# Optimization experiments

Hardware: AMD Instinct MI355X
Metric: run time of the kernel (lower is better)

The kernel has to match this reference:

```python
import jax, jax.numpy as jnp
import numpy as np

N_EMBD = 1024
N_HEAD = 16
HEAD_DIM = N_EMBD // N_HEAD
MASK_FILL = -10.0  # module uses -10, not -inf


def setup_inputs() -> dict:
    key = jax.random.key(0)
    kx, kq, kk, kv, ko = jax.random.split(key, 5)
    B, T = 4, 2048
    s = 1.0 / np.sqrt(N_EMBD)
    return {
        "x": jax.random.normal(kx, (B, T, N_EMBD), dtype=jnp.float32),
        "wq": jax.random.normal(kq, (N_EMBD, N_EMBD), dtype=jnp.float32) * s,
        "wk": jax.random.normal(kk, (N_EMBD, N_EMBD), dtype=jnp.float32) * s,
        "wv": jax.random.normal(kv, (N_EMBD, N_EMBD), dtype=jnp.float32) * s,
        "wo": jax.random.normal(ko, (N_EMBD, N_EMBD), dtype=jnp.float32) * s,
    }


def reference(x, wq, wk, wv, wo):
    B, T, C = x.shape
    # nn.Linear applies x @ W.T; weights here stored as [out, in]
    q = (x @ wq.T).reshape(B, T, N_HEAD, HEAD_DIM).transpose(0, 2, 1, 3)
    k = (x @ wk.T).reshape(B, T, N_HEAD, HEAD_DIM).transpose(0, 2, 1, 3)
    v = (x @ wv.T).reshape(B, T, N_HEAD, HEAD_DIM).transpose(0, 2, 1, 3)
    scale = 1.0 / np.sqrt(HEAD_DIM)
    att = jnp.einsum("bhqd,bhkd->bhqk", q, k) * scale  # [B,H,T,T]
    causal = jnp.tril(jnp.ones((T, T), dtype=bool))
    att = jnp.where(causal[None, None, :, :], att, MASK_FILL)
    att = jax.nn.softmax(att, axis=-1)
    y = jnp.einsum("bhqk,bhkd->bhqd", att, v)
    y = y.transpose(0, 2, 1, 3).reshape(B, T, C)
    return y @ wo.T
```

## Files before the change

kernel.cpp:

```cpp
#include <hip/hip_runtime.h>

typedef __attribute__((ext_vector_type(8))) short bf16x8;
typedef __attribute__((ext_vector_type(4))) float f32x4;

#define T_SEQ 2048
#define EXPM10 4.5399929762484854e-05f

__device__ __forceinline__ unsigned short f2bf(float f) {
    unsigned int u = __builtin_bit_cast(unsigned int, f);
    u += 0x7fffu + ((u >> 16) & 1u);
    return (unsigned short)(u >> 16);
}
__device__ __forceinline__ float bf2f(unsigned short u) {
    return __builtin_bit_cast(float, (unsigned int)u << 16);
}

__device__ __forceinline__ void async16(void* lds, const void* g) {
    __builtin_amdgcn_global_load_lds(
        (__attribute__((address_space(1))) void*)g,
        (__attribute__((address_space(3))) void*)lds, 16, 0, 0);
}

__global__ __launch_bounds__(256) void cvt_bf16(const float* __restrict__ src,
                                                unsigned short* __restrict__ dst, int n4) {
    int i = blockIdx.x * 256 + threadIdx.x;
    if (i < n4) {
        float4 v = ((const float4*)src)[i];
        ushort4 r;
        r.x = f2bf(v.x); r.y = f2bf(v.y); r.z = f2bf(v.z); r.w = f2bf(v.w);
        ((ushort4*)dst)[i] = r;
    }
}

__global__ __launch_bounds__(256) void cvt_w(const float* __restrict__ wq,
                                             const float* __restrict__ wk,
                                             const float* __restrict__ wv,
                                             const float* __restrict__ wo,
                                             unsigned short* __restrict__ wqkv,
                                             unsigned short* __restrict__ wob) {
    int which = blockIdx.x >> 10;
    int i = (blockIdx.x & 1023) * 256 + threadIdx.x;
    const float* src = which == 0 ? wq : which == 1 ? wk : which == 2 ? wv : wo;
    unsigned short* dst = which < 3 ? wqkv + (size_t)which * 1048576 : wob;
    float4 v = ((const float4*)src)[i];
    ushort4 r;
    r.x = f2bf(v.x); r.y = f2bf(v.y); r.z = f2bf(v.z); r.w = f2bf(v.w);
    ((ushort4*)dst)[i] = r;
}

__global__ __launch_bounds__(256) void gemm_qkv(const unsigned short* __restrict__ A,
                                                const unsigned short* __restrict__ B,
                                                unsigned short* __restrict__ Qb,
                                                unsigned short* __restrict__ Kb,
                                                unsigned short* __restrict__ Vtb) {
    __shared__ unsigned short As[128 * 32];
    __shared__ unsigned short Bs[128 * 32];
    const int K = 1024;
    int m0 = blockIdx.y * 128, n0 = blockIdx.x * 128;
    int tid = threadIdx.x;
    int wave = tid >> 6, lane = tid & 63;
    int r = lane & 15, q = lane >> 4;
    int wr = wave >> 1, wc = wave & 1;

    f32x4 acc[4][4];
#pragma unroll
    for (int i = 0; i < 4; i++)
#pragma unroll
        for (int j = 0; j < 4; j++) acc[i][j] = (f32x4){0.f, 0.f, 0.f, 0.f};

    for (int k0 = 0; k0 < K; k0 += 32) {
#pragma unroll
        for (int i = 0; i < 2; i++) {
            int li = i * 256 + tid;
            int row = li >> 2, kk = (li & 3) << 3;
            async16(&As[i * 2048 + wave * 512], &A[(size_t)(m0 + row) * K + k0 + kk]);
            async16(&Bs[i * 2048 + wave * 512], &B[(size_t)(n0 + row) * K + k0 + kk]);
        }
        __syncthreads();
        bf16x8 af[4], bfr[4];
#pragma unroll
        for (int mi = 0; mi < 4; mi++)
            af[mi] = *(const bf16x8*)&As[(wr * 64 + mi * 16 + r) * 32 + q * 8];
#pragma unroll
        for (int ni = 0; ni < 4; ni++)
            bfr[ni] = *(const bf16x8*)&Bs[(wc * 64 + ni * 16 + r) * 32 + q * 8];
#pragma unroll
        for (int mi = 0; mi < 4; mi++)
#pragma unroll
            for (int ni = 0; ni < 4; ni++)
                acc[mi][ni] = __builtin_amdgcn_mfma_f32_16x16x32_bf16(
                    af[mi], bfr[ni], acc[mi][ni], 0, 0, 0);
        __syncthreads();
    }

#pragma unroll
    for (int mi = 0; mi < 4; mi++) {
#pragma unroll
        for (int ni = 0; ni < 4; ni++) {
#pragma unroll
            for (int rr = 0; rr < 4; rr++) {
                int gm = m0 + wr * 64 + mi * 16 + q * 4 + rr;
                int gn = n0 + wc * 64 + ni * 16 + r;
                float v = acc[mi][ni][rr];
                int b = gm >> 11, t = gm & 2047;
                int sel = gn >> 10, nn = gn & 1023;
                int h = nn >> 6, d = nn & 63;
                if (sel == 0)
                    Qb[((size_t)(b * 16 + h) * 2048 + t) * 64 + d] = f2bf(v);
                else if (sel == 1)
                    Kb[((size_t)(b * 16 + h) * 2048 + t) * 64 + d] = f2bf(v);
                else
                    Vtb[((size_t)(b * 16 + h) * 64 + d) * 2048 + t] = f2bf(v);
            }
        }
    }
}

__global__ __launch_bounds__(256) void gemm_out(const unsigned short* __restrict__ A,
                                                const unsigned short* __restrict__ B,
                                                float* __restrict__ out) {
    __shared__ unsigned short As[128 * 32];
    __shared__ unsigned short Bs[128 * 32];
    const int K = 1024;
    int m0 = blockIdx.y * 128, n0 = blockIdx.x * 128;
    int tid = threadIdx.x;
    int wave = tid >> 6, lane = tid & 63;
    int r = lane & 15, q = lane >> 4;
    int wr = wave >> 1, wc = wave & 1;

    f32x4 acc[4][4];
#pragma unroll
    for (int i = 0; i < 4; i++)
#pragma unroll
        for (int j = 0; j < 4; j++) acc[i][j] = (f32x4){0.f, 0.f, 0.f, 0.f};

    for (int k0 = 0; k0 < K; k0 += 32) {
#pragma unroll
        for (int i = 0; i < 2; i++) {
            int li = i * 256 + tid;
            int row = li >> 2, kk = (li & 3) << 3;
            async16(&As[i * 2048 + wave * 512], &A[(size_t)(m0 + row) * K + k0 + kk]);
            async16(&Bs[i * 2048 + wave * 512], &B[(size_t)(n0 + row) * K + k0 + kk]);
        }
        __syncthreads();
        bf16x8 af[4], bfr[4];
#pragma unroll
        for (int mi = 0; mi < 4; mi++)
            af[mi] = *(const bf16x8*)&As[(wr * 64 + mi * 16 + r) * 32 + q * 8];
#pragma unroll
        for (int ni = 0; ni < 4; ni++)
            bfr[ni] = *(const bf16x8*)&Bs[(wc * 64 + ni * 16 + r) * 32 + q * 8];
#pragma unroll
        for (int mi = 0; mi < 4; mi++)
#pragma unroll
            for (int ni = 0; ni < 4; ni++)
                acc[mi][ni] = __builtin_amdgcn_mfma_f32_16x16x32_bf16(
                    af[mi], bfr[ni], acc[mi][ni], 0, 0, 0);
        __syncthreads();
    }

#pragma unroll
    for (int mi = 0; mi < 4; mi++)
#pragma unroll
        for (int ni = 0; ni < 4; ni++)
#pragma unroll
            for (int rr = 0; rr < 4; rr++) {
                int gm = m0 + wr * 64 + mi * 16 + q * 4 + rr;
                int gn = n0 + wc * 64 + ni * 16 + r;
                out[(size_t)gm * 1024 + gn] = acc[mi][ni][rr];
            }
}

__global__ __launch_bounds__(256) void suffix_sv(const unsigned short* __restrict__ Vt,
                                                 float* __restrict__ SV) {
    __shared__ float bsum[32][64];
    int bh = blockIdx.x;
    int d = threadIdx.x & 63, c = threadIdx.x >> 6;
    const unsigned short* base = Vt + ((size_t)bh * 64 + d) * T_SEQ;
#pragma unroll
    for (int jj = 0; jj < 8; jj++) {
        int j = c * 8 + jj;
        float s = 0.f;
#pragma unroll
        for (int t8 = 0; t8 < 8; t8++) {
            bf16x8 v = *(const bf16x8*)(base + j * 64 + t8 * 8);
#pragma unroll
            for (int e = 0; e < 8; e++) s += bf2f((unsigned short)v[e]);
        }
        bsum[j][d] = s;
    }
    __syncthreads();
    if (threadIdx.x < 64) {
        float run = 0.f;
        for (int j = 31; j >= 0; j--) {
            run += bsum[j][d];
            SV[((size_t)bh * 32 + j) * 64 + d] = run;
        }
    }
}

#define KST 72
#define VST 72
#define PST 72
__global__ __launch_bounds__(256) void attn(const unsigned short* __restrict__ Q,
                                            const unsigned short* __restrict__ Kg,
                                            const unsigned short* __restrict__ Vt,
                                            const float* __restrict__ SV,
                                            unsigned short* __restrict__ Y) {
    __shared__ unsigned short Ks[64 * KST];
    __shared__ unsigned short Vs[64 * VST];
    __shared__ unsigned short Ps[4][16 * PST];
    int bh = blockIdx.y;
    int qi = 31 - blockIdx.x;
    int q0 = qi * 64;
    int tid = threadIdx.x, wave = tid >> 6, lane = tid & 63;
    int r = lane & 15, qd = lane >> 4;
    int query = q0 + wave * 16 + r;

    const unsigned short* qptr = Q + ((size_t)bh * T_SEQ + query) * 64 + qd * 8;
    bf16x8 qf0 = *(const bf16x8*)qptr;
    bf16x8 qf1 = *(const bf16x8*)(qptr + 32);

    float l_lane = 0.0f;
    f32x4 o[4];
#pragma unroll
    for (int n = 0; n < 4; n++) o[n] = (f32x4){0.f, 0.f, 0.f, 0.f};

    int srow = tid >> 2, scol = (tid & 3) * 16;
    const unsigned short* kg = Kg + ((size_t)bh * T_SEQ + srow) * 64 + scol;
    const unsigned short* vg = Vt + ((size_t)bh * 64 + srow) * T_SEQ + scol;
    const float scale = 0.125f;

    bf16x8 pk0 = *(const bf16x8*)(kg);
    bf16x8 pk1 = *(const bf16x8*)(kg + 8);
    bf16x8 pv0 = *(const bf16x8*)(vg);
    bf16x8 pv1 = *(const bf16x8*)(vg + 8);

    int iters = qi + 1;
    for (int it = 0; it < iters; ++it) {
        __syncthreads();
        *(bf16x8*)&Ks[srow * KST + scol]     = pk0;
        *(bf16x8*)&Ks[srow * KST + scol + 8] = pk1;
        *(bf16x8*)&Vs[srow * VST + scol]     = pv0;
        *(bf16x8*)&Vs[srow * VST + scol + 8] = pv1;
        __syncthreads();
        if (it + 1 < iters) {
            size_t kn = (size_t)(it + 1) * 64;
            pk0 = *(const bf16x8*)(kg + kn * 64);
            pk1 = *(const bf16x8*)(kg + kn * 64 + 8);
            pv0 = *(const bf16x8*)(vg + kn);
            pv1 = *(const bf16x8*)(vg + kn + 8);
        }

        int k0 = it * 64;
        f32x4 st[4];
#pragma unroll
        for (int t = 0; t < 4; t++) {
            bf16x8 kf0 = *(const bf16x8*)&Ks[(t * 16 + r) * KST + qd * 8];
            bf16x8 kf1 = *(const bf16x8*)&Ks[(t * 16 + r) * KST + 32 + qd * 8];
            st[t] = (f32x4){0.f, 0.f, 0.f, 0.f};
            st[t] = __builtin_amdgcn_mfma_f32_16x16x32_bf16(kf0, qf0, st[t], 0, 0, 0);
            st[t] = __builtin_amdgcn_mfma_f32_16x16x32_bf16(kf1, qf1, st[t], 0, 0, 0);
        }

        float p[4][4], sum = 0.f;
        bool anymask = (k0 + 63 > q0 + wave * 16);
        if (anymask) {
#pragma unroll
            for (int t = 0; t < 4; t++)
#pragma unroll
                for (int e = 0; e < 4; e++) {
                    int kgidx = k0 + t * 16 + qd * 4 + e;
                    float pe = __expf(st[t][e] * scale);
                    p[t][e] = (kgidx <= query) ? pe : EXPM10;
                    sum += p[t][e];
                }
        } else {
#pragma unroll
            for (int t = 0; t < 4; t++)
#pragma unroll
                for (int e = 0; e < 4; e++) {
                    p[t][e] = __expf(st[t][e] * scale);
                    sum += p[t][e];
                }
        }
        l_lane += sum;

#pragma unroll
        for (int t = 0; t < 4; t++) {
            ushort4 pk;
            pk.x = f2bf(p[t][0]); pk.y = f2bf(p[t][1]);
            pk.z = f2bf(p[t][2]); pk.w = f2bf(p[t][3]);
            *(ushort4*)&Ps[wave][r * PST + t * 16 + qd * 4] = pk;
        }
        __builtin_amdgcn_sched_barrier(0);

        bf16x8 pf0 = *(const bf16x8*)&Ps[wave][r * PST + qd * 8];
        bf16x8 pf1 = *(const bf16x8*)&Ps[wave][r * PST + 32 + qd * 8];
#pragma unroll
        for (int n = 0; n < 4; n++) {
            bf16x8 vf0 = *(const bf16x8*)&Vs[(n * 16 + r) * VST + qd * 8];
            bf16x8 vf1 = *(const bf16x8*)&Vs[(n * 16 + r) * VST + 32 + qd * 8];
            o[n] = __builtin_amdgcn_mfma_f32_16x16x32_bf16(vf0, pf0, o[n], 0, 0, 0);
            o[n] = __builtin_amdgcn_mfma_f32_16x16x32_bf16(vf1, pf1, o[n], 0, 0, 0);
        }
    }

    float l_i = l_lane;
    l_i += __shfl_xor(l_i, 16);
    l_i += __shfl_xor(l_i, 32);

    float pm = 0.f, tail_l = 0.f;
    float sv[4][4];
#pragma unroll
    for (int n = 0; n < 4; n++)
#pragma unroll
        for (int e = 0; e < 4; e++) sv[n][e] = 0.f;
    if (qi < 31) {
        pm = EXPM10;
        tail_l = (float)(T_SEQ - 64 * (qi + 1)) * pm;
        const float* svp = SV + ((size_t)bh * 32 + qi + 1) * 64;
#pragma unroll
        for (int n = 0; n < 4; n++) {
            float4 f = *(const float4*)(svp + n * 16 + qd * 4);
            sv[n][0] = f.x; sv[n][1] = f.y; sv[n][2] = f.z; sv[n][3] = f.w;
        }
    }
    float inv = 1.0f / (l_i + tail_l);
    int b = bh >> 4, h = bh & 15;
#pragma unroll
    for (int n = 0; n < 4; n++) {
        ushort4 yk;
        yk.x = f2bf((o[n][0] + pm * sv[n][0]) * inv);
        yk.y = f2bf((o[n][1] + pm * sv[n][1]) * inv);
        yk.z = f2bf((o[n][2] + pm * sv[n][2]) * inv);
        yk.w = f2bf((o[n][3] + pm * sv[n][3]) * inv);
        *(ushort4*)&Y[(((size_t)b * T_SEQ + query) * 16 + h) * 64 + n * 16 + qd * 4] = yk;
    }
}

extern "C" void kernel_launch(void* const* d_in, const int* in_sizes, int n_in,
                              void* d_out, int out_size, void* d_ws, size_t ws_size,
                              hipStream_t stream) {
    const float* x  = (const float*)d_in[0];
    const float* wq = (const float*)d_in[1];
    const float* wk = (const float*)d_in[2];
    const float* wv = (const float*)d_in[3];
    const float* wo = (const float*)d_in[4];

    char* ws = (char*)d_ws;
    const size_t MB = 1u << 20;
    unsigned short* xb   = (unsigned short*)(ws);
    unsigned short* Qb   = (unsigned short*)(ws + 16 * MB);
    unsigned short* Kb   = (unsigned short*)(ws + 32 * MB);
    unsigned short* Vtb  = (unsigned short*)(ws + 48 * MB);
    unsigned short* wqkv = (unsigned short*)(ws + 64 * MB);
    unsigned short* wob  = (unsigned short*)(ws + 70 * MB);
    unsigned short* Yb   = xb;
    float* SVf = (float*)d_out;

    cvt_bf16<<<8192, 256, 0, stream>>>(x, xb, 2097152);
    cvt_w<<<4096, 256, 0, stream>>>(wq, wk, wv, wo, wqkv, wob);

    gemm_qkv<<<dim3(24, 64), 256, 0, stream>>>(xb, wqkv, Qb, Kb, Vtb);

    suffix_sv<<<64, 256, 0, stream>>>(Vtb, SVf);

    attn<<<dim3(32, 64), 256, 0, stream>>>(Qb, Kb, Vtb, SVf, Yb);

    gemm_out<<<dim3(8, 64), 256, 0, stream>>>(Yb, wob, (float*)d_out);
}
```

Measured before the change: 349.6 us.

## Double query tile per attention block and widen GEMM K-step to 64

The attention kernel now processes 128 queries per block as two 64-query groups, so each K/V tile loaded into shared memory serves twice as many queries. This halves the grid and reuses K/V staging, with the first group skipping the final diagonal tile. Both GEMMs now stage two 32-wide K slices per barrier pair, halving synchronisation count. The trade-offs are more registers and LDS per block, and fewer blocks for the causal attention grid, which can hurt occupancy and load balance.

```diff
diff --git a/kernel.cpp b/kernel.cpp
--- a/kernel.cpp
+++ b/kernel.cpp
@@ -53,8 +53,8 @@
                                                 unsigned short* __restrict__ Qb,
                                                 unsigned short* __restrict__ Kb,
                                                 unsigned short* __restrict__ Vtb) {
-    __shared__ unsigned short As[128 * 32];
-    __shared__ unsigned short Bs[128 * 32];
+    __shared__ unsigned short As[2][4096];
+    __shared__ unsigned short Bs[2][4096];
     const int K = 1024;
     int m0 = blockIdx.y * 128, n0 = blockIdx.x * 128;
     int tid = threadIdx.x;
@@ -68,28 +68,34 @@
 #pragma unroll
         for (int j = 0; j < 4; j++) acc[i][j] = (f32x4){0.f, 0.f, 0.f, 0.f};
 
-    for (int k0 = 0; k0 < K; k0 += 32) {
-#pragma unroll
-        for (int i = 0; i < 2; i++) {
-            int li = i * 256 + tid;
-            int row = li >> 2, kk = (li & 3) << 3;
-            async16(&As[i * 2048 + wave * 512], &A[(size_t)(m0 + row) * K + k0 + kk]);
-            async16(&Bs[i * 2048 + wave * 512], &B[(size_t)(n0 + row) * K + k0 + kk]);
-        }
-        __syncthreads();
-        bf16x8 af[4], bfr[4];
-#pragma unroll
-        for (int mi = 0; mi < 4; mi++)
-            af[mi] = *(const bf16x8*)&As[(wr * 64 + mi * 16 + r) * 32 + q * 8];
-#pragma unroll
-        for (int ni = 0; ni < 4; ni++)
-            bfr[ni] = *(const bf16x8*)&Bs[(wc * 64 + ni * 16 + r) * 32 + q * 8];
-#pragma unroll
-        for (int mi = 0; mi < 4; mi++)
+    int row = tid >> 2, kk = (tid & 3) << 3;
+    for (int k0 = 0; k0 < K; k0 += 64) {
+#pragma unroll
+        for (int s = 0; s < 2; s++)
+#pragma unroll
+            for (int i = 0; i < 2; i++) {
+                int li = i * 256 + tid;
+                int rw = li >> 2, kc = (li & 3) << 3;
+                async16(&As[s][i * 2048 + wave * 512], &A[(size_t)(m0 + rw) * K + k0 + s * 32 + kc]);
+                async16(&Bs[s][i * 2048 + wave * 512], &B[(size_t)(n0 + rw) * K + k0 + s * 32 + kc]);
+            }
+        __syncthreads();
+#pragma unroll
+        for (int s = 0; s < 2; s++) {
+            bf16x8 af[4], bfr[4];
+#pragma unroll
+            for (int mi = 0; mi < 4; mi++)
+                af[mi] = *(const bf16x8*)&As[s][(wr * 64 + mi * 16 + r) * 32 + q * 8];
 #pragma unroll
             for (int ni = 0; ni < 4; ni++)
-                acc[mi][ni] = __builtin_amdgcn_mfma_f32_16x16x32_bf16(
-                    af[mi], bfr[ni], acc[mi][ni], 0, 0, 0);
+                bfr[ni] = *(const bf16x8*)&Bs[s][(wc * 64 + ni * 16 + r) * 32 + q * 8];
+#pragma unroll
+            for (int mi = 0; mi < 4; mi++)
+#pragma unroll
+                for (int ni = 0; ni < 4; ni++)
+                    acc[mi][ni] = __builtin_amdgcn_mfma_f32_16x16x32_bf16(
+                        af[mi], bfr[ni], acc[mi][ni], 0, 0, 0);
+        }
         __syncthreads();
     }
 
@@ -119,8 +125,8 @@
 __global__ __launch_bounds__(256) void gemm_out(const unsigned short* __restrict__ A,
                                                 const unsigned short* __restrict__ B,
                                                 float* __restrict__ out) {
-    __shared__ unsigned short As[128 * 32];
-    __shared__ unsigned short Bs[128 * 32];
+    __shared__ unsigned short As[2][4096];
+    __shared__ unsigned short Bs[2][4096];
     const int K = 1024;
     int m0 = blockIdx.y * 128, n0 = blockIdx.x * 128;
     int tid = threadIdx.x;
@@ -134,28 +140,33 @@
 #pragma unroll
         for (int j = 0; j < 4; j++) acc[i][j] = (f32x4){0.f, 0.f, 0.f, 0.f};
 
-    for (int k0 = 0; k0 < K; k0 += 32) {
-#pragma unroll
-        for (int i = 0; i < 2; i++) {
-            int li = i * 256 + tid;
-            int row = li >> 2, kk = (li & 3) << 3;
-            async16(&As[i * 2048 + wave * 512], &A[(size_t)(m0 + row) * K + k0 + kk]);
-            async16(&Bs[i * 2048 + wave * 512], &B[(size_t)(n0 + row) * K + k0 + kk]);
-        }
-        __syncthreads();
-        bf16x8 af[4], bfr[4];
-#pragma unroll
-        for (int mi = 0; mi < 4; mi++)
-            af[mi] = *(const bf16x8*)&As[(wr * 64 + mi * 16 + r) * 32 + q * 8];
-#pragma unroll
-        for (int ni = 0; ni < 4; ni++)
-            bfr[ni] = *(const bf16x8*)&Bs[(wc * 64 + ni * 16 + r) * 32 + q * 8];
-#pragma unroll
-        for (int mi = 0; mi < 4; mi++)
+    for (int k0 = 0; k0 < K; k0 += 64) {
+#pragma unroll
+        for (int s = 0; s < 2; s++)
+#pragma unroll
+            for (int i = 0; i < 2; i++) {
+                int li = i * 256 + tid;
+                int rw = li >> 2, kc = (li & 3) << 3;
+                async16(&As[s][i * 2048 + wave * 512], &A[(size_t)(m0 + rw) * K + k0 + s * 32 + kc]);
+                async16(&Bs[s][i * 2048 + wave * 512], &B[(size_t)(n0 + rw) * K + k0 + s * 32 + kc]);
+            }
+        __syncthreads();
+#pragma unroll
+        for (int s = 0; s < 2; s++) {
+            bf16x8 af[4], bfr[4];
+#pragma unroll
+            for (int mi = 0; mi < 4; mi++)
+                af[mi] = *(const bf16x8*)&As[s][(wr * 64 + mi * 16 + r) * 32 + q * 8];
 #pragma unroll
             for (int ni = 0; ni < 4; ni++)
-                acc[mi][ni] = __builtin_amdgcn_mfma_f32_16x16x32_bf16(
-                    af[mi], bfr[ni], acc[mi][ni], 0, 0, 0);
+                bfr[ni] = *(const bf16x8*)&Bs[s][(wc * 64 + ni * 16 + r) * 32 + q * 8];
+#pragma unroll
+            for (int mi = 0; mi < 4; mi++)
+#pragma unroll
+                for (int ni = 0; ni < 4; ni++)
+                    acc[mi][ni] = __builtin_amdgcn_mfma_f32_16x16x32_bf16(
+                        af[mi], bfr[ni], acc[mi][ni], 0, 0, 0);
+        }
         __syncthreads();
     }
 
@@ -209,35 +220,42 @@
                                             unsigned short* __restrict__ Y) {
     __shared__ unsigned short Ks[64 * KST];
     __shared__ unsigned short Vs[64 * VST];
-    __shared__ unsigned short Ps[4][16 * PST];
+    __shared__ unsigned short Ps[8 * 16 * PST];
     int bh = blockIdx.y;
-    int qi = 31 - blockIdx.x;
-    int q0 = qi * 64;
+    int qi = 15 - blockIdx.x;
+    int q0 = qi * 128;
     int tid = threadIdx.x, wave = tid >> 6, lane = tid & 63;
     int r = lane & 15, qd = lane >> 4;
-    int query = q0 + wave * 16 + r;
-
-    const unsigned short* qptr = Q + ((size_t)bh * T_SEQ + query) * 64 + qd * 8;
-    bf16x8 qf0 = *(const bf16x8*)qptr;
-    bf16x8 qf1 = *(const bf16x8*)(qptr + 32);
-
-    float l_lane = 0.0f;
-    f32x4 o[4];
-#pragma unroll
-    for (int n = 0; n < 4; n++) o[n] = (f32x4){0.f, 0.f, 0.f, 0.f};
+    int query0 = q0 + wave * 16 + r;
+    int query1 = query0 + 64;
+
+    const unsigned short* qptr = Q + ((size_t)bh * T_SEQ + query0) * 64 + qd * 8;
+    bf16x8 qf00 = *(const bf16x8*)qptr;
+    bf16x8 qf01 = *(const bf16x8*)(qptr + 32);
+    bf16x8 qf10 = *(const bf16x8*)(qptr + 64 * 64);
+    bf16x8 qf11 = *(const bf16x8*)(qptr + 64 * 64 + 32);
+
+    float l0 = 0.f, l1 = 0.f;
+    f32x4 o0[4], o1[4];
+#pragma unroll
+    for (int n = 0; n < 4; n++) { o0[n] = (f32x4){0.f,0.f,0.f,0.f}; o1[n] = o0[n]; }
 
     int srow = tid >> 2, scol = (tid & 3) * 16;
     const unsigned short* kg = Kg + ((size_t)bh * T_SEQ + srow) * 64 + scol;
     const unsigned short* vg = Vt + ((size_t)bh * 64 + srow) * T_SEQ + scol;
     const float scale = 0.125f;
 
+    unsigned short* ps0 = &Ps[(wave * 2 + 0) * 16 * PST];
+    unsigned short* ps1 = &Ps[(wave * 2 + 1) * 16 * PST];
+
     bf16x8 pk0 = *(const bf16x8*)(kg);
     bf16x8 pk1 = *(const bf16x8*)(kg + 8);
     bf16x8 pv0 = *(const bf16x8*)(vg);
     bf16x8 pv1 = *(const bf16x8*)(vg + 8);
 
-    int iters = qi + 1;
+    int iters = 2 * qi + 2;
     for (int it = 0; it < iters; ++it) {
+        bool g0run = (it < iters - 1);
         __syncthreads();
         *(bf16x8*)&Ks[srow * KST + scol]     = pk0;
         *(bf16x8*)&Ks[srow * KST + scol + 8] = pk1;
@@ -253,89 +271,126 @@
         }
 
         int k0 = it * 64;
-        f32x4 st[4];
+        f32x4 st0[4], st1[4];
 #pragma unroll
         for (int t = 0; t < 4; t++) {
             bf16x8 kf0 = *(const bf16x8*)&Ks[(t * 16 + r) * KST + qd * 8];
             bf16x8 kf1 = *(const bf16x8*)&Ks[(t * 16 + r) * KST + 32 + qd * 8];
-            st[t] = (f32x4){0.f, 0.f, 0.f, 0.f};
-            st[t] = __builtin_amdgcn_mfma_f32_16x16x32_bf16(kf0, qf0, st[t], 0, 0, 0);
-            st[t] = __builtin_amdgcn_mfma_f32_16x16x32_bf16(kf1, qf1, st[t], 0, 0, 0);
-        }
-
-        float p[4][4], sum = 0.f;
-        bool anymask = (k0 + 63 > q0 + wave * 16);
-        if (anymask) {
-#pragma unroll
-            for (int t = 0; t < 4; t++)
-#pragma unroll
-                for (int e = 0; e < 4; e++) {
-                    int kgidx = k0 + t * 16 + qd * 4 + e;
-                    float pe = __expf(st[t][e] * scale);
-                    p[t][e] = (kgidx <= query) ? pe : EXPM10;
-                    sum += p[t][e];
+            if (g0run) {
+                st0[t] = (f32x4){0.f,0.f,0.f,0.f};
+                st0[t] = __builtin_amdgcn_mfma_f32_16x16x32_bf16(kf0, qf00, st0[t], 0, 0, 0);
+                st0[t] = __builtin_amdgcn_mfma_f32_16x16x32_bf16(kf1, qf01, st0[t], 0, 0, 0);
+            }
+            st1[t] = (f32x4){0.f,0.f,0.f,0.f};
+            st1[t] = __builtin_amdgcn_mfma_f32_16x16x32_bf16(kf0, qf10, st1[t], 0, 0, 0);
+            st1[t] = __builtin_amdgcn_mfma_f32_16x16x32_bf16(kf1, qf11, st1[t], 0, 0, 0);
+        }
+
+        if (g0run) {
+            float sum = 0.f;
+            bool anymask = (k0 + 63 > q0 + wave * 16);
+#pragma unroll
+            for (int t = 0; t < 4; t++) {
+                float p[4];
+                if (anymask) {
+#pragma unroll
+                    for (int e = 0; e < 4; e++) {
+                        int kgidx = k0 + t * 16 + qd * 4 + e;
+                        float pe = __expf(st0[t][e] * scale);
+                        p[e] = (kgidx <= query0) ? pe : EXPM10;
+                        sum += p[e];
+                    }
+                } else {
+#pragma unroll
+                    for (int e = 0; e < 4; e++) { p[e] = __expf(st0[t][e] * scale); sum += p[e]; }
                 }
-        } else {
-#pragma unroll
-            for (int t = 0; t < 4; t++)
-#pragma unroll
-                for (int e = 0; e < 4; e++) {
-                    p[t][e] = __expf(st[t][e] * scale);
-                    sum += p[t][e];
+                ushort4 pk;
+                pk.x = f2bf(p[0]); pk.y = f2bf(p[1]); pk.z = f2bf(p[2]); pk.w = f2bf(p[3]);
+                *(ushort4*)&ps0[r * PST + t * 16 + qd * 4] = pk;
+            }
+            l0 += sum;
+        }
+        {
+            float sum = 0.f;
+            bool anymask = (k0 + 63 > q0 + 64 + wave * 16);
+#pragma unroll
+            for (int t = 0; t < 4; t++) {
+                float p[4];
+                if (anymask) {
+#pragma unroll
+                    for (int e = 0; e < 4; e++) {
+                        int kgidx = k0 + t * 16 + qd * 4 + e;
+                        float pe = __expf(st1[t][e] * scale);
+                        p[e] = (kgidx <= query1) ? pe : EXPM10;
+                        sum += p[e];
+                    }
+                } else {
+#pragma unroll
+                    for (int e = 0; e < 4; e++) { p[e] = __expf(st1[t][e] * scale); sum += p[e]; }
                 }
-        }
-        l_lane += sum;
-
-#pragma unroll
-        for (int t = 0; t < 4; t++) {
-            ushort4 pk;
-            pk.x = f2bf(p[t][0]); pk.y = f2bf(p[t][1]);
-            pk.z = f2bf(p[t][2]); pk.w = f2bf(p[t][3]);
-            *(ushort4*)&Ps[wave][r * PST + t * 16 + qd * 4] = pk;
+                ushort4 pk;
+                pk.x = f2bf(p[0]); pk.y = f2bf(p[1]); pk.z = f2bf(p[2]); pk.w = f2bf(p[3]);
+                *(ushort4*)&ps1[r * PST + t * 16 + qd * 4] = pk;
+            }
+            l1 += sum;
         }
         __builtin_amdgcn_sched_barrier(0);
 
-        bf16x8 pf0 = *(const bf16x8*)&Ps[wave][r * PST + qd * 8];
-        bf16x8 pf1 = *(const bf16x8*)&Ps[wave][r * PST + 32 + qd * 8];
+        bf16x8 pf00, pf01, pf10, pf11;
+        if (g0run) {
+            pf00 = *(const bf16x8*)&ps0[r * PST + qd * 8];
+            pf01 = *(const bf16x8*)&ps0[r * PST + 32 + qd * 8];
+        }
+        pf10 = *(const bf16x8*)&ps1[r * PST + qd * 8];
+        pf11 = *(const bf16x8*)&ps1[r * PST + 32 + qd * 8];
 #pragma unroll
         for (int n = 0; n < 4; n++) {
             bf16x8 vf0 = *(const bf16x8*)&Vs[(n * 16 + r) * VST + qd * 8];
             bf16x8 vf1 = *(const bf16x8*)&Vs[(n * 16 + r) * VST + 32 + qd * 8];
-            o[n] = __builtin_amdgcn_mfma_f32_16x16x32_bf16(vf0, pf0, o[n], 0, 0, 0);
-            o[n] = __builtin_amdgcn_mfma_f32_16x16x32_bf16(vf1, pf1, o[n], 0, 0, 0);
-        }
-    }
-
-    float l_i = l_lane;
-    l_i += __shfl_xor(l_i, 16);
-    l_i += __shfl_xor(l_i, 32);
-
-    float pm = 0.f, tail_l = 0.f;
-    float sv[4][4];
-#pragma unroll
-    for (int n = 0; n < 4; n++)
-#pragma unroll
-        for (int e = 0; e < 4; e++) sv[n][e] = 0.f;
-    if (qi < 31) {
-        pm = EXPM10;
-        tail_l = (float)(T_SEQ - 64 * (qi + 1)) * pm;
-        const float* svp = SV + ((size_t)bh * 32 + qi + 1) * 64;
+            if (g0run) {
+                o0[n] = __builtin_amdgcn_mfma_f32_16x16x32_bf16(vf0, pf00, o0[n], 0, 0, 0);
+                o0[n] = __builtin_amdgcn_mfma_f32_16x16x32_bf16(vf1, pf01, o0[n], 0, 0, 0);
+            }
+            o1[n] = __builtin_amdgcn_mfma_f32_16x16x32_bf16(vf0, pf10, o1[n], 0, 0, 0);
+            o1[n] = __builtin_amdgcn_mfma_f32_16x16x32_bf16(vf1, pf11, o1[n], 0, 0, 0);
+        }
+    }
+
+    int b = bh >> 4, h = bh & 15;
+#pragma unroll
+    for (int g = 0; g < 2; g++) {
+        float l_i = g == 0 ? l0 : l1;
+        l_i += __shfl_xor(l_i, 16);
+        l_i += __shfl_xor(l_i, 32);
+        int j = 2 * qi + g + 1;
+        int query = g == 0 ? query0 : query1;
+        f32x4* o = g == 0 ? o0 : o1;
+        float pm = 0.f, tail_l = 0.f;
+        float sv[4][4];
+#pragma unroll
+        for (int n = 0; n < 4; n++)
+#pragma unroll
+            for (int e = 0; e < 4; e++) sv[n][e] = 0.f;
+        if (j < 32) {
+            pm = EXPM10;
+            tail_l = (float)(T_SEQ - 64 * j) * pm;
+            const float* svp = SV + ((size_t)bh * 32 + j) * 64;
+#pragma unroll
+            for (int n = 0; n < 4; n++) {
+                float4 f = *(const float4*)(svp + n * 16 + qd * 4);
+                sv[n][0] = f.x; sv[n][1] = f.y; sv[n][2] = f.z; sv[n][3] = f.w;
+            }
+        }
+        float inv = 1.0f / (l_i + tail_l);
 #pragma unroll
         for (int n = 0; n < 4; n++) {
-            float4 f = *(const float4*)(svp + n * 16 + qd * 4);
-            sv[n][0] = f.x; sv[n][1] = f.y; sv[n][2] = f.z; sv[n][3] = f.w;
-        }
-    }
-    float inv = 1.0f / (l_i + tail_l);
-    int b = bh >> 4, h = bh & 15;
-#pragma unroll
-    for (int n = 0; n < 4; n++) {
-        ushort4 yk;
-        yk.x = f2bf((o[n][0] + pm * sv[n][0]) * inv);
-        yk.y = f2bf((o[n][1] + pm * sv[n][1]) * inv);
-        yk.z = f2bf((o[n][2] + pm * sv[n][2]) * inv);
-        yk.w = f2bf((o[n][3] + pm * sv[n][3]) * inv);
-        *(ushort4*)&Y[(((size_t)b * T_SEQ + query) * 16 + h) * 64 + n * 16 + qd * 4] = yk;
+            ushort4 yk;
+            yk.x = f2bf((o[n][0] + pm * sv[n][0]) * inv);
+            yk.y = f2bf((o[n][1] + pm * sv[n][1]) * inv);
+            yk.z = f2bf((o[n][2] + pm * sv[n][2]) * inv);
+            yk.w = f2bf((o[n][3] + pm * sv[n][3]) * inv);
+            *(ushort4*)&Y[(((size_t)b * T_SEQ + query) * 16 + h) * 64 + n * 16 + qd * 4] = yk;
+        }
     }
 }
 
@@ -366,7 +421,7 @@
 
     suffix_sv<<<64, 256, 0, stream>>>(Vtb, SVf);
 
-    attn<<<dim3(32, 64), 256, 0, stream>>>(Qb, Kb, Vtb, SVf, Yb);
+    attn<<<dim3(16, 64), 256, 0, stream>>>(Qb, Kb, Vtb, SVf, Yb);
 
     gemm_out<<<dim3(8, 64), 256, 0, stream>>>(Yb, wob, (float*)d_out);
 }
```

Result: slower. 363.9 us (+4.1%).

## Read K/V directly from global in attention and double k-step per GEMM sync

Applied to the files above, without the earlier changes.

The attention kernel drops the shared-memory staging of K and V tiles and the two block-wide barriers per iteration. Each wave now loads its K and V MFMA fragments straight from global memory and relies on L1/L2 reuse across the four waves. The loop bound is kept the same (g+1 tiles), and the softmax loop is restructured so P is written to LDS per tile. Separately, both GEMMs now load two 32-wide k-slices per barrier pair, which halves the synchronisation count at the cost of twice the LDS.

```diff
diff --git a/kernel.cpp b/kernel.cpp
--- a/kernel.cpp
+++ b/kernel.cpp
@@ -53,8 +53,8 @@
                                                 unsigned short* __restrict__ Qb,
                                                 unsigned short* __restrict__ Kb,
                                                 unsigned short* __restrict__ Vtb) {
-    __shared__ unsigned short As[128 * 32];
-    __shared__ unsigned short Bs[128 * 32];
+    __shared__ unsigned short As[2][4096];
+    __shared__ unsigned short Bs[2][4096];
     const int K = 1024;
     int m0 = blockIdx.y * 128, n0 = blockIdx.x * 128;
     int tid = threadIdx.x;
@@ -68,28 +68,33 @@
 #pragma unroll
         for (int j = 0; j < 4; j++) acc[i][j] = (f32x4){0.f, 0.f, 0.f, 0.f};
 
-    for (int k0 = 0; k0 < K; k0 += 32) {
-#pragma unroll
-        for (int i = 0; i < 2; i++) {
-            int li = i * 256 + tid;
-            int row = li >> 2, kk = (li & 3) << 3;
-            async16(&As[i * 2048 + wave * 512], &A[(size_t)(m0 + row) * K + k0 + kk]);
-            async16(&Bs[i * 2048 + wave * 512], &B[(size_t)(n0 + row) * K + k0 + kk]);
-        }
+    for (int k0 = 0; k0 < K; k0 += 64) {
+#pragma unroll
+        for (int s = 0; s < 2; s++)
+#pragma unroll
+            for (int i = 0; i < 2; i++) {
+                int li = i * 256 + tid;
+                int rw = li >> 2, kc = (li & 3) << 3;
+                async16(&As[s][i * 2048 + wave * 512], &A[(size_t)(m0 + rw) * K + k0 + s * 32 + kc]);
+                async16(&Bs[s][i * 2048 + wave * 512], &B[(size_t)(n0 + rw) * K + k0 + s * 32 + kc]);
+            }
         __syncthreads();
-        bf16x8 af[4], bfr[4];
-#pragma unroll
-        for (int mi = 0; mi < 4; mi++)
-            af[mi] = *(const bf16x8*)&As[(wr * 64 + mi * 16 + r) * 32 + q * 8];
-#pragma unroll
-        for (int ni = 0; ni < 4; ni++)
-            bfr[ni] = *(const bf16x8*)&Bs[(wc * 64 + ni * 16 + r) * 32 + q * 8];
-#pragma unroll
-        for (int mi = 0; mi < 4; mi++)
+#pragma unroll
+        for (int s = 0; s < 2; s++) {
+            bf16x8 af[4], bfr[4];
+#pragma unroll
+            for (int mi = 0; mi < 4; mi++)
+                af[mi] = *(const bf16x8*)&As[s][(wr * 64 + mi * 16 + r) * 32 + q * 8];
 #pragma unroll
             for (int ni = 0; ni < 4; ni++)
-                acc[mi][ni] = __builtin_amdgcn_mfma_f32_16x16x32_bf16(
-                    af[mi], bfr[ni], acc[mi][ni], 0, 0, 0);
+                bfr[ni] = *(const bf16x8*)&Bs[s][(wc * 64 + ni * 16 + r) * 32 + q * 8];
+#pragma unroll
+            for (int mi = 0; mi < 4; mi++)
+#pragma unroll
+                for (int ni = 0; ni < 4; ni++)
+                    acc[mi][ni] = __builtin_amdgcn_mfma_f32_16x16x32_bf16(
+                        af[mi], bfr[ni], acc[mi][ni], 0, 0, 0);
+        }
         __syncthreads();
     }
 
@@ -119,8 +124,8 @@
 __global__ __launch_bounds__(256) void gemm_out(const unsigned short* __restrict__ A,
                                                 const unsigned short* __restrict__ B,
                                                 float* __restrict__ out) {
-    __shared__ unsigned short As[128 * 32];
-    __shared__ unsigned short Bs[128 * 32];
+    __shared__ unsigned short As[2][4096];
+    __shared__ unsigned short Bs[2][4096];
     const int K = 1024;
     int m0 = blockIdx.y * 128, n0 = blockIdx.x * 128;
     int tid = threadIdx.x;
@@ -134,28 +139,33 @@
 #pragma unroll
         for (int j = 0; j < 4; j++) acc[i][j] = (f32x4){0.f, 0.f, 0.f, 0.f};
 
-    for (int k0 = 0; k0 < K; k0 += 32) {
-#pragma unroll
-        for (int i = 0; i < 2; i++) {
-            int li = i * 256 + tid;
-            int row = li >> 2, kk = (li & 3) << 3;
-            async16(&As[i * 2048 + wave * 512], &A[(size_t)(m0 + row) * K + k0 + kk]);
-            async16(&Bs[i * 2048 + wave * 512], &B[(size_t)(n0 + row) * K + k0 + kk]);
-        }
+    for (int k0 = 0; k0 < K; k0 += 64) {
+#pragma unroll
+        for (int s = 0; s < 2; s++)
+#pragma unroll
+            for (int i = 0; i < 2; i++) {
+                int li = i * 256 + tid;
+                int rw = li >> 2, kc = (li & 3) << 3;
+                async16(&As[s][i * 2048 + wave * 512], &A[(size_t)(m0 + rw) * K + k0 + s * 32 + kc]);
+                async16(&Bs[s][i * 2048 + wave * 512], &B[(size_t)(n0 + rw) * K + k0 + s * 32 + kc]);
+            }
         __syncthreads();
-        bf16x8 af[4], bfr[4];
-#pragma unroll
-        for (int mi = 0; mi < 4; mi++)
-            af[mi] = *(const bf16x8*)&As[(wr * 64 + mi * 16 + r) * 32 + q * 8];
-#pragma unroll
-        for (int ni = 0; ni < 4; ni++)
-            bfr[ni] = *(const bf16x8*)&Bs[(wc * 64 + ni * 16 + r) * 32 + q * 8];
-#pragma unroll
-        for (int mi = 0; mi < 4; mi++)
+#pragma unroll
+        for (int s = 0; s < 2; s++) {
+            bf16x8 af[4], bfr[4];
+#pragma unroll
+            for (int mi = 0; mi < 4; mi++)
+                af[mi] = *(const bf16x8*)&As[s][(wr * 64 + mi * 16 + r) * 32 + q * 8];
 #pragma unroll
             for (int ni = 0; ni < 4; ni++)
-                acc[mi][ni] = __builtin_amdgcn_mfma_f32_16x16x32_bf16(
-                    af[mi], bfr[ni], acc[mi][ni], 0, 0, 0);
+                bfr[ni] = *(const bf16x8*)&Bs[s][(wc * 64 + ni * 16 + r) * 32 + q * 8];
+#pragma unroll
+            for (int mi = 0; mi < 4; mi++)
+#pragma unroll
+                for (int ni = 0; ni < 4; ni++)
+                    acc[mi][ni] = __builtin_amdgcn_mfma_f32_16x16x32_bf16(
+                        af[mi], bfr[ni], acc[mi][ni], 0, 0, 0);
+        }
         __syncthreads();
     }
 
@@ -199,108 +209,83 @@
     }
 }
 
-#define KST 72
-#define VST 72
 #define PST 72
 __global__ __launch_bounds__(256) void attn(const unsigned short* __restrict__ Q,
                                             const unsigned short* __restrict__ Kg,
                                             const unsigned short* __restrict__ Vt,
                                             const float* __restrict__ SV,
                                             unsigned short* __restrict__ Y) {
-    __shared__ unsigned short Ks[64 * KST];
-    __shared__ unsigned short Vs[64 * VST];
     __shared__ unsigned short Ps[4][16 * PST];
     int bh = blockIdx.y;
-    int qi = 31 - blockIdx.x;
-    int q0 = qi * 64;
+    int g = 31 - blockIdx.x;
     int tid = threadIdx.x, wave = tid >> 6, lane = tid & 63;
     int r = lane & 15, qd = lane >> 4;
-    int query = q0 + wave * 16 + r;
+    int s = 4 * g + wave;
+    int query = 16 * s + r;
 
     const unsigned short* qptr = Q + ((size_t)bh * T_SEQ + query) * 64 + qd * 8;
     bf16x8 qf0 = *(const bf16x8*)qptr;
     bf16x8 qf1 = *(const bf16x8*)(qptr + 32);
 
-    float l_lane = 0.0f;
+    const unsigned short* kbase = Kg + (size_t)bh * T_SEQ * 64;
+    const unsigned short* vbase = Vt + (size_t)bh * 64 * T_SEQ;
+    const float scale = 0.125f;
+
+    float l_lane = 0.f;
     f32x4 o[4];
 #pragma unroll
     for (int n = 0; n < 4; n++) o[n] = (f32x4){0.f, 0.f, 0.f, 0.f};
 
-    int srow = tid >> 2, scol = (tid & 3) * 16;
-    const unsigned short* kg = Kg + ((size_t)bh * T_SEQ + srow) * 64 + scol;
-    const unsigned short* vg = Vt + ((size_t)bh * 64 + srow) * T_SEQ + scol;
-    const float scale = 0.125f;
-
-    bf16x8 pk0 = *(const bf16x8*)(kg);
-    bf16x8 pk1 = *(const bf16x8*)(kg + 8);
-    bf16x8 pv0 = *(const bf16x8*)(vg);
-    bf16x8 pv1 = *(const bf16x8*)(vg + 8);
-
-    int iters = qi + 1;
-    for (int it = 0; it < iters; ++it) {
-        __syncthreads();
-        *(bf16x8*)&Ks[srow * KST + scol]     = pk0;
-        *(bf16x8*)&Ks[srow * KST + scol + 8] = pk1;
-        *(bf16x8*)&Vs[srow * VST + scol]     = pv0;
-        *(bf16x8*)&Vs[srow * VST + scol + 8] = pv1;
-        __syncthreads();
-        if (it + 1 < iters) {
-            size_t kn = (size_t)(it + 1) * 64;
-            pk0 = *(const bf16x8*)(kg + kn * 64);
-            pk1 = *(const bf16x8*)(kg + kn * 64 + 8);
-            pv0 = *(const bf16x8*)(vg + kn);
-            pv1 = *(const bf16x8*)(vg + kn + 8);
-        }
-
+    for (int it = 0; it <= g; ++it) {
         int k0 = it * 64;
         f32x4 st[4];
 #pragma unroll
         for (int t = 0; t < 4; t++) {
-            bf16x8 kf0 = *(const bf16x8*)&Ks[(t * 16 + r) * KST + qd * 8];
-            bf16x8 kf1 = *(const bf16x8*)&Ks[(t * 16 + r) * KST + 32 + qd * 8];
+            const unsigned short* kp = kbase + (size_t)(k0 + t * 16 + r) * 64 + qd * 8;
+            bf16x8 kf0 = *(const bf16x8*)kp;
+            bf16x8 kf1 = *(const bf16x8*)(kp + 32);
             st[t] = (f32x4){0.f, 0.f, 0.f, 0.f};
             st[t] = __builtin_amdgcn_mfma_f32_16x16x32_bf16(kf0, qf0, st[t], 0, 0, 0);
             st[t] = __builtin_amdgcn_mfma_f32_16x16x32_bf16(kf1, qf1, st[t], 0, 0, 0);
         }
 
-        float p[4][4], sum = 0.f;
-        bool anymask = (k0 + 63 > q0 + wave * 16);
-        if (anymask) {
-#pragma unroll
-            for (int t = 0; t < 4; t++)
+        float sum = 0.f;
+        if (it == g) {
+#pragma unroll
+            for (int t = 0; t < 4; t++) {
+                float p[4];
 #pragma unroll
                 for (int e = 0; e < 4; e++) {
                     int kgidx = k0 + t * 16 + qd * 4 + e;
                     float pe = __expf(st[t][e] * scale);
-                    p[t][e] = (kgidx <= query) ? pe : EXPM10;
-                    sum += p[t][e];
+                    p[e] = (kgidx <= query) ? pe : EXPM10;
+                    sum += p[e];
                 }
+                ushort4 pk;
+                pk.x = f2bf(p[0]); pk.y = f2bf(p[1]); pk.z = f2bf(p[2]); pk.w = f2bf(p[3]);
+                *(ushort4*)&Ps[wave][r * PST + t * 16 + qd * 4] = pk;
+            }
         } else {
 #pragma unroll
-            for (int t = 0; t < 4; t++)
-#pragma unroll
-                for (int e = 0; e < 4; e++) {
-                    p[t][e] = __expf(st[t][e] * scale);
-                    sum += p[t][e];
-                }
+            for (int t = 0; t < 4; t++) {
+                float p[4];
+#pragma unroll
+                for (int e = 0; e < 4; e++) { p[e] = __expf(st[t][e] * scale); sum += p[e]; }
+                ushort4 pk;
+                pk.x = f2bf(p[0]); pk.y = f2bf(p[1]); pk.z = f2bf(p[2]); pk.w = f2bf(p[3]);
+                *(ushort4*)&Ps[wave][r * PST + t * 16 + qd * 4] = pk;
+            }
         }
         l_lane += sum;
-
-#pragma unroll
-        for (int t = 0; t < 4; t++) {
-            ushort4 pk;
-            pk.x = f2bf(p[t][0]); pk.y = f2bf(p[t][1]);
-            pk.z = f2bf(p[t][2]); pk.w = f2bf(p[t][3]);
-            *(ushort4*)&Ps[wave][r * PST + t * 16 + qd * 4] = pk;
-        }
         __builtin_amdgcn_sched_barrier(0);
 
         bf16x8 pf0 = *(const bf16x8*)&Ps[wave][r * PST + qd * 8];
         bf16x8 pf1 = *(const bf16x8*)&Ps[wave][r * PST + 32 + qd * 8];
 #pragma unroll
         for (int n = 0; n < 4; n++) {
-            bf16x8 vf0 = *(const bf16x8*)&Vs[(n * 16 + r) * VST + qd * 8];
-            bf16x8 vf1 = *(const bf16x8*)&Vs[(n * 16 + r) * VST + 32 + qd * 8];
+            const unsigned short* vp = vbase + (size_t)(n * 16 + r) * T_SEQ + k0 + qd * 8;
+            bf16x8 vf0 = *(const bf16x8*)vp;
+            bf16x8 vf1 = *(const bf16x8*)(vp + 32);
             o[n] = __builtin_amdgcn_mfma_f32_16x16x32_bf16(vf0, pf0, o[n], 0, 0, 0);
             o[n] = __builtin_amdgcn_mfma_f32_16x16x32_bf16(vf1, pf1, o[n], 0, 0, 0);
         }
@@ -310,16 +295,17 @@
     l_i += __shfl_xor(l_i, 16);
     l_i += __shfl_xor(l_i, 32);
 
+    int j = g + 1;
     float pm = 0.f, tail_l = 0.f;
     float sv[4][4];
 #pragma unroll
     for (int n = 0; n < 4; n++)
 #pragma unroll
         for (int e = 0; e < 4; e++) sv[n][e] = 0.f;
-    if (qi < 31) {
+    if (j < 32) {
         pm = EXPM10;
-        tail_l = (float)(T_SEQ - 64 * (qi + 1)) * pm;
-        const float* svp = SV + ((size_t)bh * 32 + qi + 1) * 64;
+        tail_l = (float)(T_SEQ - 64 * j) * pm;
+        const float* svp = SV + ((size_t)bh * 32 + j) * 64;
 #pragma unroll
         for (int n = 0; n < 4; n++) {
             float4 f = *(const float4*)(svp + n * 16 + qd * 4);
```

Result: slower. 676.5 us (+93.5%).
